# Performance work log

Measured on AMD Instinct MI355X. Metric: run time of the kernel, lower is better.

The kernel has to match this reference:

```python
import jax, jax.numpy as jnp
import numpy as np

D_IN = 4096
NUM_HEADS = 32
NUM_KV_GROUPS = 8
HEAD_DIM = D_IN // NUM_HEADS  # 128 (init overwrites head_dim)
GROUP_SIZE = NUM_HEADS // NUM_KV_GROUPS
SEQ = 2048
BATCH = 1
EPS = 1e-6


def layernorm(t, w, b):
    mu = jnp.mean(t, axis=-1, keepdims=True)
    var = jnp.var(t, axis=-1, keepdims=True)
    return (t - mu) * jax.lax.rsqrt(var + EPS) * w + b


def rope(t, cos, sin):
    # t: [B, H, S, D]; cos/sin: [S, D] broadcast over B, H
    half = t.shape[-1] // 2
    x1, x2 = t[..., :half], t[..., half:]
    rot = jnp.concatenate([-x2, x1], axis=-1)
    return t * cos + rot * sin


def setup_inputs() -> dict:
    key = jax.random.key(0)
    ks = jax.random.split(key, 10)
    x = jax.random.normal(ks[0], (BATCH, SEQ, D_IN), dtype=jnp.float32)
    mask = jnp.triu(jnp.ones((SEQ, SEQ), dtype=bool), k=1)  # True = masked (causal)
    # RoPE tables
    inv_freq = 1.0 / (10000.0 ** (np.arange(0, HEAD_DIM, 2, dtype=np.float32) / HEAD_DIM))
    pos = np.arange(SEQ, dtype=np.float32)
    ang = np.einsum('s,d->sd', pos, inv_freq)  # [S, D/2]
    ang = np.concatenate([ang, ang], axis=-1)  # [S, D]
    cos = jnp.asarray(np.cos(ang))
    sin = jnp.asarray(np.sin(ang))
    s = 0.02
    Wq = jax.random.normal(ks[1], (D_IN, NUM_HEADS * HEAD_DIM), dtype=jnp.float32) * s
    Wk = jax.random.normal(ks[2], (D_IN, NUM_KV_GROUPS * HEAD_DIM), dtype=jnp.float32) * s
    Wv = jax.random.normal(ks[3], (D_IN, NUM_KV_GROUPS * HEAD_DIM), dtype=jnp.float32) * s
    Wo = jax.random.normal(ks[4], (NUM_HEADS * HEAD_DIM, D_IN), dtype=jnp.float32) * s
    qn_w = jnp.ones((HEAD_DIM,), jnp.float32)
    qn_b = jnp.zeros((HEAD_DIM,), jnp.float32)
    kn_w = jnp.ones((HEAD_DIM,), jnp.float32)
    kn_b = jnp.zeros((HEAD_DIM,), jnp.float32)
    return {"x": x, "mask": mask, "cos": cos, "sin": sin, "Wq": Wq, "Wk": Wk,
            "Wv": Wv, "Wo": Wo, "qn_w": qn_w, "qn_b": qn_b, "kn_w": kn_w, "kn_b": kn_b}


def reference(x, mask, cos, sin, Wq, Wk, Wv, Wo, qn_w, qn_b, kn_w, kn_b):
    B, S, _ = x.shape
    q = (x @ Wq).reshape(B, S, NUM_HEADS, HEAD_DIM).transpose(0, 2, 1, 3)      # [B,H,S,D]
    k = (x @ Wk).reshape(B, S, NUM_KV_GROUPS, HEAD_DIM).transpose(0, 2, 1, 3)  # [B,G,S,D]
    v = (x @ Wv).reshape(B, S, NUM_KV_GROUPS, HEAD_DIM).transpose(0, 2, 1, 3)
    q = layernorm(q, qn_w, qn_b)
    k = layernorm(k, kn_w, kn_b)
    q = rope(q, cos, sin)
    k = rope(k, cos, sin)
    k = jnp.repeat(k, GROUP_SIZE, axis=1)  # [B,H,S,D]
    v = jnp.repeat(v, GROUP_SIZE, axis=1)
    scores = jnp.einsum('bhqd,bhkd->bhqk', q, k)
    scores = jnp.where(mask, -jnp.inf, scores)
    attn = jax.nn.softmax(scores / jnp.sqrt(jnp.float32(HEAD_DIM)), axis=-1)
    ctx = jnp.einsum('bhqk,bhkd->bhqd', attn, v)
    ctx = ctx.transpose(0, 2, 1, 3).reshape(B, S, NUM_HEADS * HEAD_DIM)
    return ctx @ Wo
```

## Files before the change

kernel.cpp:

```cpp
#include <hip/hip_runtime.h>
#include <stdint.h>

#define SQ   2048
#define DIN  4096
#define NH   32
#define NKV  8
#define HD   128
#define NQKV 6144

typedef float f32x4 __attribute__((ext_vector_type(4)));
typedef short bf16x8 __attribute__((ext_vector_type(8)));

__device__ __forceinline__ short f2bf(float f) {
  union { float f; uint32_t u; } v; v.f = f;
  uint32_t r = (v.u + 0x7FFFu + ((v.u >> 16) & 1u)) >> 16;
  return (short)r;
}

__device__ __forceinline__ void gl2lds(const void* g, void* l) {
  __builtin_amdgcn_global_load_lds(
      (const __attribute__((address_space(1))) void*)g,
      (__attribute__((address_space(3))) void*)l, 16, 0, 0);
}

__global__ void cvt_bf16(const float* __restrict__ src, short* __restrict__ dst, long n) {
  long i = ((long)blockIdx.x * blockDim.x + threadIdx.x) * 4;
  if (i + 3 < n) {
    float4 v = *(const float4*)(src + i);
    short o[4] = { f2bf(v.x), f2bf(v.y), f2bf(v.z), f2bf(v.w) };
    *(uint2*)(dst + i) = *(uint2*)o;
  }
}

__global__ __launch_bounds__(256) void transpose_cvt(const float* __restrict__ src, int ldS, long zS,
                                                     short* __restrict__ dst, int ldD, long zD) {
  __shared__ float tile[64][65];
  src += (long)blockIdx.z * zS;
  dst += (long)blockIdx.z * zD;
  int r0 = blockIdx.y * 64, c0 = blockIdx.x * 64;
  int tid = threadIdx.x;
#pragma unroll
  for (int i = 0; i < 16; ++i) {
    int idx = i * 256 + tid;
    int rr = idx >> 6, cc = idx & 63;
    tile[rr][cc] = src[(long)(r0 + rr) * ldS + c0 + cc];
  }
  __syncthreads();
#pragma unroll
  for (int i = 0; i < 16; ++i) {
    int idx = i * 256 + tid;
    int dr = idx >> 6, dc = idx & 63;
    dst[(long)(c0 + dr) * ldD + r0 + dc] = f2bf(tile[dc][dr]);
  }
}

#define BM 128
#define BN 128
#define BK 32
__global__ __launch_bounds__(256) void gemm_bf16(const short* __restrict__ A, const short* __restrict__ Bt,
                                                 float* __restrict__ C, int M, int N, int K) {
  __shared__ __align__(16) short As[BM * BK];
  __shared__ __align__(16) short Bs[BN * BK];
  int tid = threadIdx.x;
  int wave = tid >> 6, lane = tid & 63;
  int l16 = lane & 15, lq = lane >> 4;
  int m0 = blockIdx.y * BM, n0 = blockIdx.x * BN;
  int wm = (wave >> 1) * 64, wn = (wave & 1) * 64;
  int ch = (lane & 3) ^ ((lane >> 3) & 3);
  f32x4 acc[4][4] = {};
  for (int k0 = 0; k0 < K; k0 += BK) {
#pragma unroll
    for (int c = 0; c < 2; ++c) {
      int call = wave * 2 + c;
      int r = call * 16 + (lane >> 2);
      gl2lds(&A[(long)(m0 + r) * K + k0 + ch * 8], &As[call * 512]);
      gl2lds(&Bt[(long)(n0 + r) * K + k0 + ch * 8], &Bs[call * 512]);
    }
    __syncthreads();
    bf16x8 af[4], bfr[4];
#pragma unroll
    for (int i = 0; i < 4; ++i) {
      int row = wm + i * 16 + l16;
      af[i] = *(const bf16x8*)&As[row * BK + (lq ^ ((row >> 1) & 3)) * 8];
    }
#pragma unroll
    for (int j = 0; j < 4; ++j) {
      int row = wn + j * 16 + l16;
      bfr[j] = *(const bf16x8*)&Bs[row * BK + (lq ^ ((row >> 1) & 3)) * 8];
    }
#pragma unroll
    for (int i = 0; i < 4; ++i)
#pragma unroll
      for (int j = 0; j < 4; ++j)
        acc[i][j] = __builtin_amdgcn_mfma_f32_16x16x32_bf16(af[i], bfr[j], acc[i][j], 0, 0, 0);
    __syncthreads();
  }
#pragma unroll
  for (int i = 0; i < 4; ++i)
#pragma unroll
    for (int j = 0; j < 4; ++j)
#pragma unroll
      for (int r = 0; r < 4; ++r) {
        int row = m0 + wm + i * 16 + lq * 4 + r;
        int col = n0 + wn + j * 16 + l16;
        C[(long)row * N + col] = acc[i][j][r];
      }
}

__global__ __launch_bounds__(64) void ln_rope(const float* __restrict__ qkv,
                                              const float* __restrict__ cosb, const float* __restrict__ sinb,
                                              const float* __restrict__ qw, const float* __restrict__ qb,
                                              const float* __restrict__ kw, const float* __restrict__ kb,
                                              short* __restrict__ qo, short* __restrict__ ko) {
  int s = blockIdx.x, slice = blockIdx.y, t = threadIdx.x;
  bool isq = slice < NH;
  int off = isq ? slice * HD : DIN + (slice - NH) * HD;
  const float* src = qkv + (long)s * NQKV + off;
  float v0 = src[t], v1 = src[t + 64];
  float sum = v0 + v1, ss = v0 * v0 + v1 * v1;
#pragma unroll
  for (int o = 1; o < 64; o <<= 1) { sum += __shfl_xor(sum, o); ss += __shfl_xor(ss, o); }
  float mu = sum * (1.f / 128.f);
  float var = ss * (1.f / 128.f) - mu * mu;
  float rstd = rsqrtf(var + 1e-6f);
  const float* w  = isq ? qw : kw;
  const float* bb = isq ? qb : kb;
  float n0 = (v0 - mu) * rstd * w[t]      + bb[t];
  float n1 = (v1 - mu) * rstd * w[t + 64] + bb[t + 64];
  float c0 = cosb[s * HD + t], c1 = cosb[s * HD + t + 64];
  float s0 = sinb[s * HD + t], s1 = sinb[s * HD + t + 64];
  float o0 = n0 * c0 - n1 * s0;
  float o1 = n1 * c1 + n0 * s1;
  short* dst = isq ? (qo + ((long)slice * SQ + s) * HD)
                   : (ko + ((long)(slice - NH) * SQ + s) * HD);
  dst[t] = f2bf(o0);
  dst[t + 64] = f2bf(o1);
}

__global__ __launch_bounds__(256) void attn(const short* __restrict__ q, const short* __restrict__ k,
                                            const short* __restrict__ vT, short* __restrict__ ctx) {
  int pair = blockIdx.x, h = blockIdx.y, g = h >> 2;
  int tid = threadIdx.x, w = tid >> 6, lane = tid & 63;
  int l16 = lane & 15, lq = lane >> 4;
  __shared__ __align__(16) short Ks[64 * 128];
  __shared__ __align__(16) short Vs[128 * 64];
  __shared__ __align__(16) short pbuf[4][16 * 72];
  const short* qh = q + (long)h * SQ * HD;
  const short* kg = k + (long)g * SQ * HD;
  const short* vg = vT + (long)g * HD * SQ;
  int kr = (w * 4) * 4 + (lane >> 4);
  int vrw = (w * 4) * 8 + (lane >> 3);
  const float sc = 0.08838834764831845f * 1.4426950408889634f;

  for (int st = 0; st < 2; ++st) {
    int qt = st ? (31 - pair) : pair;
    int qbase = qt * 64 + w * 16;
    bf16x8 aq[4];
#pragma unroll
    for (int kk = 0; kk < 4; ++kk)
      aq[kk] = *(const bf16x8*)&qh[(long)(qbase + l16) * HD + kk * 32 + lq * 8];
    float m_r[4], l_r[4];
    f32x4 acc[8] = {};
#pragma unroll
    for (int r = 0; r < 4; ++r) { m_r[r] = -__builtin_inff(); l_r[r] = 0.f; }

    for (int kt = 0; kt <= qt; ++kt) {
#pragma unroll
      for (int j = 0; j < 4; ++j) {
        int call = w * 4 + j;
        int r = kr + j * 4;
        int chk = (lane & 15) ^ (r & 15);
        gl2lds(&kg[(long)(kt * 64 + r) * HD + chk * 8], &Ks[call * 512]);
        int rv = vrw + j * 8;
        int chv = (lane & 7) ^ (rv & 7);
        gl2lds(&vg[(long)rv * SQ + kt * 64 + chv * 8], &Vs[call * 512]);
      }
      __syncthreads();
      f32x4 s4[4];
#pragma unroll
      for (int b = 0; b < 4; ++b) s4[b] = (f32x4){0.f, 0.f, 0.f, 0.f};
#pragma unroll
      for (int b = 0; b < 4; ++b) {
        int krow = b * 16 + l16;
#pragma unroll
        for (int kk = 0; kk < 4; ++kk) {
          bf16x8 bk = *(const bf16x8*)&Ks[krow * 128 + ((kk * 4 + lq) ^ (krow & 15)) * 8];
          s4[b] = __builtin_amdgcn_mfma_f32_16x16x32_bf16(aq[kk], bk, s4[b], 0, 0, 0);
        }
      }
      int qrow0 = qbase + lq * 4;
#pragma unroll
      for (int b = 0; b < 4; ++b) {
        int key = kt * 64 + b * 16 + l16;
#pragma unroll
        for (int r = 0; r < 4; ++r) {
          float val = s4[b][r] * sc;
          s4[b][r] = (key > qrow0 + r) ? -__builtin_inff() : val;
        }
      }
      float p[4][4];
#pragma unroll
      for (int r = 0; r < 4; ++r) {
        float mx = fmaxf(fmaxf(s4[0][r], s4[1][r]), fmaxf(s4[2][r], s4[3][r]));
#pragma unroll
        for (int o = 1; o < 16; o <<= 1) mx = fmaxf(mx, __shfl_xor(mx, o));
        float mnew = fmaxf(m_r[r], mx);
        float alpha = exp2f(m_r[r] - mnew);
        float sum = 0.f;
#pragma unroll
        for (int b = 0; b < 4; ++b) { float pv = exp2f(s4[b][r] - mnew); p[b][r] = pv; sum += pv; }
#pragma unroll
        for (int o = 1; o < 16; o <<= 1) sum += __shfl_xor(sum, o);
        l_r[r] = l_r[r] * alpha + sum;
        m_r[r] = mnew;
#pragma unroll
        for (int n = 0; n < 8; ++n) acc[n][r] *= alpha;
      }
#pragma unroll
      for (int b = 0; b < 4; ++b)
#pragma unroll
        for (int r = 0; r < 4; ++r)
          pbuf[w][(lq * 4 + r) * 72 + b * 16 + l16] = f2bf(p[b][r]);
#pragma unroll
      for (int kk = 0; kk < 2; ++kk) {
        bf16x8 pf = *(const bf16x8*)&pbuf[w][l16 * 72 + kk * 32 + lq * 8];
#pragma unroll
        for (int n = 0; n < 8; ++n) {
          int vrow = n * 16 + l16;
          bf16x8 vf = *(const bf16x8*)&Vs[vrow * 64 + ((kk * 4 + lq) ^ (vrow & 7)) * 8];
          acc[n] = __builtin_amdgcn_mfma_f32_16x16x32_bf16(pf, vf, acc[n], 0, 0, 0);
        }
      }
      __syncthreads();
    }
#pragma unroll
    for (int n = 0; n < 8; ++n)
#pragma unroll
      for (int r = 0; r < 4; ++r) {
        int srow = qbase + lq * 4 + r;
        ctx[(long)srow * (NH * HD) + h * HD + n * 16 + l16] = f2bf(acc[n][r] / l_r[r]);
      }
  }
}

#define XB_OFF     0L
#define QR_OFF     0L
#define WQKVT_OFF  16777216L
#define KR_OFF     16777216L
#define VT_OFF     20971520L
#define CTX_OFF    25165824L
#define WOT_OFF    67108864L
#define QKV_OFF    100663296L

extern "C" void kernel_launch(void* const* d_in, const int* in_sizes, int n_in,
                              void* d_out, int out_size, void* d_ws, size_t ws_size,
                              hipStream_t stream) {
  const float* x    = (const float*)d_in[0];
  const float* cosb = (const float*)d_in[2];
  const float* sinb = (const float*)d_in[3];
  const float* Wq   = (const float*)d_in[4];
  const float* Wk   = (const float*)d_in[5];
  const float* Wv   = (const float*)d_in[6];
  const float* Wo   = (const float*)d_in[7];
  const float* qnw  = (const float*)d_in[8];
  const float* qnb  = (const float*)d_in[9];
  const float* knw  = (const float*)d_in[10];
  const float* knb  = (const float*)d_in[11];

  char* ws = (char*)d_ws;
  short* xb    = (short*)(ws + XB_OFF);
  short* qr    = (short*)(ws + QR_OFF);
  short* wqkvt = (short*)(ws + WQKVT_OFF);
  short* krp   = (short*)(ws + KR_OFF);
  short* vt    = (short*)(ws + VT_OFF);
  short* ctx   = (short*)(ws + CTX_OFF);
  short* wot   = (short*)(ws + WOT_OFF);
  float* qkv   = (float*)(ws + QKV_OFF);

  cvt_bf16<<<8192, 256, 0, stream>>>(x, xb, (long)SQ * DIN);
  transpose_cvt<<<dim3(64, 64, 1), 256, 0, stream>>>(Wq, 4096, 0L, wqkvt, 4096, 0L);
  transpose_cvt<<<dim3(16, 64, 1), 256, 0, stream>>>(Wk, 1024, 0L, wqkvt + (long)4096 * 4096, 4096, 0L);
  transpose_cvt<<<dim3(16, 64, 1), 256, 0, stream>>>(Wv, 1024, 0L, wqkvt + (long)5120 * 4096, 4096, 0L);
  transpose_cvt<<<dim3(64, 64, 1), 256, 0, stream>>>(Wo, 4096, 0L, wot, 4096, 0L);
  gemm_bf16<<<dim3(NQKV / BN, SQ / BM), 256, 0, stream>>>(xb, wqkvt, qkv, SQ, NQKV, DIN);
  ln_rope<<<dim3(SQ, NH + NKV), 64, 0, stream>>>(qkv, cosb, sinb, qnw, qnb, knw, knb, qr, krp);
  transpose_cvt<<<dim3(2, 32, 8), 256, 0, stream>>>(qkv + 5120, NQKV, 128L, vt, SQ, (long)HD * SQ);
  attn<<<dim3(16, NH), 256, 0, stream>>>(qr, krp, vt, ctx);
  gemm_bf16<<<dim3(DIN / BN, SQ / BM), 256, 0, stream>>>(ctx, wot, (float*)d_out, SQ, DIN, DIN);
}
```

Measured before the change: 609.9 us.

## Fuse LayerNorm, RoPE and V transpose into QKV GEMM epilogue; restructure attention

```diff
diff --git a/kernel.cpp b/kernel.cpp
--- a/kernel.cpp
+++ b/kernel.cpp
@@ -57,6 +57,112 @@
 #define BM 128
 #define BN 128
 #define BK 32
+
+__global__ __launch_bounds__(256) void gemm_qkv(const short* __restrict__ A, const short* __restrict__ Bt,
+                                                const float* __restrict__ cosb, const float* __restrict__ sinb,
+                                                const float* __restrict__ qw, const float* __restrict__ qb,
+                                                const float* __restrict__ kw, const float* __restrict__ kb,
+                                                short* __restrict__ qo, short* __restrict__ ko,
+                                                short* __restrict__ vo) {
+  __shared__ __align__(16) short smem[8704];
+  short* As = smem;
+  short* Bs = smem + 4096;
+  const int K = DIN;
+  int tid = threadIdx.x, wave = tid >> 6, lane = tid & 63;
+  int l16 = lane & 15, lq = lane >> 4;
+  int m0 = blockIdx.y * BM;
+  int cb = blockIdx.x;
+  long n0 = (long)cb * BN;
+  int wm = wave * 32;
+  int ch = (lane & 3) ^ ((lane >> 3) & 3);
+  f32x4 acc[2][8] = {};
+  for (int k0 = 0; k0 < K; k0 += BK) {
+#pragma unroll
+    for (int c = 0; c < 2; ++c) {
+      int call = wave * 2 + c;
+      int r = call * 16 + (lane >> 2);
+      gl2lds(&A[(long)(m0 + r) * K + k0 + ch * 8], &As[call * 512]);
+      gl2lds(&Bt[(n0 + r) * K + k0 + ch * 8], &Bs[call * 512]);
+    }
+    __syncthreads();
+    bf16x8 af[2], bfr[8];
+#pragma unroll
+    for (int i = 0; i < 2; ++i) {
+      int row = wm + i * 16 + l16;
+      af[i] = *(const bf16x8*)&As[row * BK + (lq ^ ((row >> 1) & 3)) * 8];
+    }
+#pragma unroll
+    for (int j = 0; j < 8; ++j) {
+      int row = j * 16 + l16;
+      bfr[j] = *(const bf16x8*)&Bs[row * BK + (lq ^ ((row >> 1) & 3)) * 8];
+    }
+#pragma unroll
+    for (int i = 0; i < 2; ++i)
+#pragma unroll
+      for (int j = 0; j < 8; ++j)
+        acc[i][j] = __builtin_amdgcn_mfma_f32_16x16x32_bf16(af[i], bfr[j], acc[i][j], 0, 0, 0);
+    __syncthreads();
+  }
+  if (cb < 40) {
+    bool isq = cb < NH;
+    const float* lw = isq ? qw : kw;
+    const float* lb = isq ? qb : kb;
+    float wv[8], bv[8];
+#pragma unroll
+    for (int j = 0; j < 8; ++j) { wv[j] = lw[j * 16 + l16]; bv[j] = lb[j * 16 + l16]; }
+    short* dst = isq ? (qo + (long)cb * SQ * HD) : (ko + (long)(cb - 32) * SQ * HD);
+#pragma unroll
+    for (int i = 0; i < 2; ++i)
+#pragma unroll
+      for (int r = 0; r < 4; ++r) {
+        int s = m0 + wm + i * 16 + lq * 4 + r;
+        float s1 = 0.f, s2 = 0.f;
+#pragma unroll
+        for (int j = 0; j < 8; ++j) { float v = acc[i][j][r]; s1 += v; s2 += v * v; }
+#pragma unroll
+        for (int o = 1; o < 16; o <<= 1) { s1 += __shfl_xor(s1, o); s2 += __shfl_xor(s2, o); }
+        float mu = s1 * (1.f / 128.f);
+        float rstd = rsqrtf(s2 * (1.f / 128.f) - mu * mu + 1e-6f);
+        float val[8];
+#pragma unroll
+        for (int j = 0; j < 8; ++j) val[j] = (acc[i][j][r] - mu) * rstd * wv[j] + bv[j];
+#pragma unroll
+        for (int j = 0; j < 4; ++j) {
+          int d = j * 16 + l16;
+          float c = cosb[(long)s * HD + d];
+          float sn = sinb[(long)s * HD + d];
+          dst[(long)s * HD + d]      = f2bf(val[j] * c - val[j + 4] * sn);
+          dst[(long)s * HD + d + 64] = f2bf(val[j + 4] * c + val[j] * sn);
+        }
+      }
+  } else {
+    short* vdst = vo + (long)(cb - 40) * HD * SQ;
+#pragma unroll
+    for (int p = 0; p < 2; ++p) {
+      __syncthreads();
+#pragma unroll
+      for (int i = 0; i < 2; ++i)
+#pragma unroll
+        for (int j = 0; j < 4; ++j) {
+          int dl = j * 16 + l16;
+#pragma unroll
+          for (int r = 0; r < 4; ++r) {
+            int sl = wm + i * 16 + lq * 4 + r;
+            smem[dl * 136 + sl] = f2bf(acc[i][p * 4 + j][r]);
+          }
+        }
+      __syncthreads();
+#pragma unroll
+      for (int c = 0; c < 4; ++c) {
+        int idx = c * 256 + tid;
+        int drow = idx >> 4, off = (idx & 15) * 8;
+        uint4 v = *(const uint4*)&smem[drow * 136 + off];
+        *(uint4*)&vdst[(long)(p * 64 + drow) * SQ + m0 + off] = v;
+      }
+    }
+  }
+}
+
 __global__ __launch_bounds__(256) void gemm_bf16(const short* __restrict__ A, const short* __restrict__ Bt,
                                                  float* __restrict__ C, int M, int N, int K) {
   __shared__ __align__(16) short As[BM * BK];
@@ -107,150 +213,149 @@
       }
 }
 
-__global__ __launch_bounds__(64) void ln_rope(const float* __restrict__ qkv,
-                                              const float* __restrict__ cosb, const float* __restrict__ sinb,
-                                              const float* __restrict__ qw, const float* __restrict__ qb,
-                                              const float* __restrict__ kw, const float* __restrict__ kb,
-                                              short* __restrict__ qo, short* __restrict__ ko) {
-  int s = blockIdx.x, slice = blockIdx.y, t = threadIdx.x;
-  bool isq = slice < NH;
-  int off = isq ? slice * HD : DIN + (slice - NH) * HD;
-  const float* src = qkv + (long)s * NQKV + off;
-  float v0 = src[t], v1 = src[t + 64];
-  float sum = v0 + v1, ss = v0 * v0 + v1 * v1;
-#pragma unroll
-  for (int o = 1; o < 64; o <<= 1) { sum += __shfl_xor(sum, o); ss += __shfl_xor(ss, o); }
-  float mu = sum * (1.f / 128.f);
-  float var = ss * (1.f / 128.f) - mu * mu;
-  float rstd = rsqrtf(var + 1e-6f);
-  const float* w  = isq ? qw : kw;
-  const float* bb = isq ? qb : kb;
-  float n0 = (v0 - mu) * rstd * w[t]      + bb[t];
-  float n1 = (v1 - mu) * rstd * w[t + 64] + bb[t + 64];
-  float c0 = cosb[s * HD + t], c1 = cosb[s * HD + t + 64];
-  float s0 = sinb[s * HD + t], s1 = sinb[s * HD + t + 64];
-  float o0 = n0 * c0 - n1 * s0;
-  float o1 = n1 * c1 + n0 * s1;
-  short* dst = isq ? (qo + ((long)slice * SQ + s) * HD)
-                   : (ko + ((long)(slice - NH) * SQ + s) * HD);
-  dst[t] = f2bf(o0);
-  dst[t + 64] = f2bf(o1);
-}
-
-__global__ __launch_bounds__(256) void attn(const short* __restrict__ q, const short* __restrict__ k,
-                                            const short* __restrict__ vT, short* __restrict__ ctx) {
+#define NEG_INF (-__builtin_inff())
+
+template<int NB, bool MASK>
+__device__ __forceinline__ void score_tile(const short* Ks, const bf16x8* aq,
+                                           float* p, float* m, float* l, f32x4* acc,
+                                           int key0, int qrow0, int l16, int lq, float sc) {
+  f32x4 s4[NB];
+#pragma unroll
+  for (int b = 0; b < NB; ++b) {
+    f32x4 t = {0.f, 0.f, 0.f, 0.f};
+#pragma unroll
+    for (int kk = 0; kk < 4; ++kk) {
+      bf16x8 bk = *(const bf16x8*)&Ks[(b * 16 + l16) * 128 + (((kk * 4 + lq) ^ l16) * 8)];
+      t = __builtin_amdgcn_mfma_f32_16x16x32_bf16(aq[kk], bk, t, 0, 0, 0);
+    }
+    if (MASK) {
+      int key = key0 + b * 16 + l16;
+#pragma unroll
+      for (int r = 0; r < 4; ++r) t[r] = (key > qrow0 + r) ? NEG_INF : t[r] * sc;
+    } else {
+#pragma unroll
+      for (int r = 0; r < 4; ++r) t[r] = t[r] * sc;
+    }
+    s4[b] = t;
+  }
+#pragma unroll
+  for (int r = 0; r < 4; ++r) {
+    float mx = s4[0][r];
+#pragma unroll
+    for (int b = 1; b < NB; ++b) mx = fmaxf(mx, s4[b][r]);
+#pragma unroll
+    for (int o = 1; o < 16; o <<= 1) mx = fmaxf(mx, __shfl_xor(mx, o));
+    float mnew = fmaxf(m[r], mx);
+    float alpha = exp2f(m[r] - mnew);
+    float sum = 0.f;
+#pragma unroll
+    for (int b = 0; b < NB; ++b) { float pv = exp2f(s4[b][r] - mnew); p[b * 4 + r] = pv; sum += pv; }
+#pragma unroll
+    for (int o = 1; o < 16; o <<= 1) sum += __shfl_xor(sum, o);
+    l[r] = l[r] * alpha + sum;
+    m[r] = mnew;
+#pragma unroll
+    for (int n = 0; n < 8; ++n) acc[n][r] *= alpha;
+  }
+}
+
+template<int NB>
+__device__ __forceinline__ void pv_tile(short* pbuf, const short* Vs, const float* p,
+                                        f32x4* acc, int l16, int lq) {
+#pragma unroll
+  for (int b = 0; b < NB; ++b)
+#pragma unroll
+    for (int r = 0; r < 4; ++r)
+      pbuf[(lq * 4 + r) * 136 + b * 16 + l16] = f2bf(p[b * 4 + r]);
+#pragma unroll
+  for (int kk = 0; kk < NB / 2; ++kk) {
+    bf16x8 pf = *(const bf16x8*)&pbuf[l16 * 136 + kk * 32 + lq * 8];
+#pragma unroll
+    for (int n = 0; n < 8; ++n) {
+      bf16x8 vf = *(const bf16x8*)&Vs[(n * 16 + l16) * 128 + (((kk * 4 + lq) ^ l16) * 8)];
+      acc[n] = __builtin_amdgcn_mfma_f32_16x16x32_bf16(pf, vf, acc[n], 0, 0, 0);
+    }
+  }
+}
+
+__global__ __launch_bounds__(256, 2) void attn(const short* __restrict__ q, const short* __restrict__ k,
+                                               const short* __restrict__ vT, short* __restrict__ ctx) {
   int pair = blockIdx.x, h = blockIdx.y, g = h >> 2;
   int tid = threadIdx.x, w = tid >> 6, lane = tid & 63;
   int l16 = lane & 15, lq = lane >> 4;
-  __shared__ __align__(16) short Ks[64 * 128];
-  __shared__ __align__(16) short Vs[128 * 64];
-  __shared__ __align__(16) short pbuf[4][16 * 72];
+  __shared__ __align__(16) short Ks[128 * 128];
+  __shared__ __align__(16) short Vs[128 * 128];
+  short* pbuf = Ks + w * 2176;
   const short* qh = q + (long)h * SQ * HD;
   const short* kg = k + (long)g * SQ * HD;
   const short* vg = vT + (long)g * HD * SQ;
-  int kr = (w * 4) * 4 + (lane >> 4);
-  int vrw = (w * 4) * 8 + (lane >> 3);
+  int qtA = pair, qtB = 31 - pair;
+  int ktmaxA = qtA >> 1, ktmaxB = qtB >> 1;
   const float sc = 0.08838834764831845f * 1.4426950408889634f;
 
-  for (int st = 0; st < 2; ++st) {
-    int qt = st ? (31 - pair) : pair;
-    int qbase = qt * 64 + w * 16;
-    bf16x8 aq[4];
-#pragma unroll
-    for (int kk = 0; kk < 4; ++kk)
-      aq[kk] = *(const bf16x8*)&qh[(long)(qbase + l16) * HD + kk * 32 + lq * 8];
-    float m_r[4], l_r[4];
-    f32x4 acc[8] = {};
-#pragma unroll
-    for (int r = 0; r < 4; ++r) { m_r[r] = -__builtin_inff(); l_r[r] = 0.f; }
-
-    for (int kt = 0; kt <= qt; ++kt) {
-#pragma unroll
-      for (int j = 0; j < 4; ++j) {
-        int call = w * 4 + j;
-        int r = kr + j * 4;
-        int chk = (lane & 15) ^ (r & 15);
-        gl2lds(&kg[(long)(kt * 64 + r) * HD + chk * 8], &Ks[call * 512]);
-        int rv = vrw + j * 8;
-        int chv = (lane & 7) ^ (rv & 7);
-        gl2lds(&vg[(long)rv * SQ + kt * 64 + chv * 8], &Vs[call * 512]);
-      }
-      __syncthreads();
-      f32x4 s4[4];
-#pragma unroll
-      for (int b = 0; b < 4; ++b) s4[b] = (f32x4){0.f, 0.f, 0.f, 0.f};
-#pragma unroll
-      for (int b = 0; b < 4; ++b) {
-        int krow = b * 16 + l16;
-#pragma unroll
-        for (int kk = 0; kk < 4; ++kk) {
-          bf16x8 bk = *(const bf16x8*)&Ks[krow * 128 + ((kk * 4 + lq) ^ (krow & 15)) * 8];
-          s4[b] = __builtin_amdgcn_mfma_f32_16x16x32_bf16(aq[kk], bk, s4[b], 0, 0, 0);
-        }
-      }
-      int qrow0 = qbase + lq * 4;
-#pragma unroll
-      for (int b = 0; b < 4; ++b) {
-        int key = kt * 64 + b * 16 + l16;
-#pragma unroll
-        for (int r = 0; r < 4; ++r) {
-          float val = s4[b][r] * sc;
-          s4[b][r] = (key > qrow0 + r) ? -__builtin_inff() : val;
-        }
-      }
-      float p[4][4];
-#pragma unroll
-      for (int r = 0; r < 4; ++r) {
-        float mx = fmaxf(fmaxf(s4[0][r], s4[1][r]), fmaxf(s4[2][r], s4[3][r]));
-#pragma unroll
-        for (int o = 1; o < 16; o <<= 1) mx = fmaxf(mx, __shfl_xor(mx, o));
-        float mnew = fmaxf(m_r[r], mx);
-        float alpha = exp2f(m_r[r] - mnew);
-        float sum = 0.f;
-#pragma unroll
-        for (int b = 0; b < 4; ++b) { float pv = exp2f(s4[b][r] - mnew); p[b][r] = pv; sum += pv; }
-#pragma unroll
-        for (int o = 1; o < 16; o <<= 1) sum += __shfl_xor(sum, o);
-        l_r[r] = l_r[r] * alpha + sum;
-        m_r[r] = mnew;
-#pragma unroll
-        for (int n = 0; n < 8; ++n) acc[n][r] *= alpha;
-      }
-#pragma unroll
-      for (int b = 0; b < 4; ++b)
-#pragma unroll
-        for (int r = 0; r < 4; ++r)
-          pbuf[w][(lq * 4 + r) * 72 + b * 16 + l16] = f2bf(p[b][r]);
-#pragma unroll
-      for (int kk = 0; kk < 2; ++kk) {
-        bf16x8 pf = *(const bf16x8*)&pbuf[w][l16 * 72 + kk * 32 + lq * 8];
-#pragma unroll
-        for (int n = 0; n < 8; ++n) {
-          int vrow = n * 16 + l16;
-          bf16x8 vf = *(const bf16x8*)&Vs[vrow * 64 + ((kk * 4 + lq) ^ (vrow & 7)) * 8];
-          acc[n] = __builtin_amdgcn_mfma_f32_16x16x32_bf16(pf, vf, acc[n], 0, 0, 0);
-        }
-      }
-      __syncthreads();
-    }
-#pragma unroll
-    for (int n = 0; n < 8; ++n)
-#pragma unroll
-      for (int r = 0; r < 4; ++r) {
-        int srow = qbase + lq * 4 + r;
-        ctx[(long)srow * (NH * HD) + h * HD + n * 16 + l16] = f2bf(acc[n][r] / l_r[r]);
-      }
-  }
+  bf16x8 aqA[4], aqB[4];
+#pragma unroll
+  for (int kk = 0; kk < 4; ++kk) {
+    aqA[kk] = *(const bf16x8*)&qh[(long)(qtA * 64 + w * 16 + l16) * HD + kk * 32 + lq * 8];
+    aqB[kk] = *(const bf16x8*)&qh[(long)(qtB * 64 + w * 16 + l16) * HD + kk * 32 + lq * 8];
+  }
+  float mA[4], lA[4], mB[4], lB[4];
+  f32x4 accA[8] = {}, accB[8] = {};
+#pragma unroll
+  for (int r = 0; r < 4; ++r) { mA[r] = NEG_INF; lA[r] = 0.f; mB[r] = NEG_INF; lB[r] = 0.f; }
+  int qrowA = qtA * 64 + w * 16 + lq * 4;
+  int qrowB = qtB * 64 + w * 16 + lq * 4;
+  float pA[32], pB[32];
+
+  for (int kt = 0; kt <= ktmaxB; ++kt) {
+    __syncthreads();
+#pragma unroll
+    for (int j = 0; j < 8; ++j) {
+      int call = w * 8 + j;
+      int r = call * 4 + (lane >> 4);
+      int chk = (lane & 15) ^ (r & 15);
+      gl2lds(&kg[(long)(kt * 128 + r) * HD + chk * 8], &Ks[call * 512]);
+      gl2lds(&vg[(long)r * SQ + kt * 128 + chk * 8], &Vs[call * 512]);
+    }
+    __syncthreads();
+    bool doA = (kt <= ktmaxA);
+    int nbB = 8, nbA = 8;
+    if (kt == ktmaxB && !(qtB & 1)) nbB = 4;
+    if (kt == ktmaxA && !(qtA & 1)) nbA = 4;
+    if (kt == ktmaxB) {
+      if (nbB == 8) score_tile<8, true>(Ks, aqB, pB, mB, lB, accB, kt * 128, qrowB, l16, lq, sc);
+      else          score_tile<4, true>(Ks, aqB, pB, mB, lB, accB, kt * 128, qrowB, l16, lq, sc);
+    } else          score_tile<8, false>(Ks, aqB, pB, mB, lB, accB, kt * 128, qrowB, l16, lq, sc);
+    if (doA) {
+      if (kt == ktmaxA) {
+        if (nbA == 8) score_tile<8, true>(Ks, aqA, pA, mA, lA, accA, kt * 128, qrowA, l16, lq, sc);
+        else          score_tile<4, true>(Ks, aqA, pA, mA, lA, accA, kt * 128, qrowA, l16, lq, sc);
+      } else          score_tile<8, false>(Ks, aqA, pA, mA, lA, accA, kt * 128, qrowA, l16, lq, sc);
+    }
+    __syncthreads();
+    if (nbB == 8) pv_tile<8>(pbuf, Vs, pB, accB, l16, lq);
+    else          pv_tile<4>(pbuf, Vs, pB, accB, l16, lq);
+    if (doA) {
+      if (nbA == 8) pv_tile<8>(pbuf, Vs, pA, accA, l16, lq);
+      else          pv_tile<4>(pbuf, Vs, pA, accA, l16, lq);
+    }
+  }
+#pragma unroll
+  for (int n = 0; n < 8; ++n)
+#pragma unroll
+    for (int r = 0; r < 4; ++r) {
+      ctx[(long)(qrowA + r) * (NH * HD) + h * HD + n * 16 + l16] = f2bf(accA[n][r] / lA[r]);
+      ctx[(long)(qrowB + r) * (NH * HD) + h * HD + n * 16 + l16] = f2bf(accB[n][r] / lB[r]);
+    }
 }
 
 #define XB_OFF     0L
-#define QR_OFF     0L
+#define CTX_OFF    0L
 #define WQKVT_OFF  16777216L
-#define KR_OFF     16777216L
-#define VT_OFF     20971520L
-#define CTX_OFF    25165824L
 #define WOT_OFF    67108864L
-#define QKV_OFF    100663296L
+#define QR_OFF     100663296L
+#define KR_OFF     117440512L
+#define VT_OFF     121634816L
 
 extern "C" void kernel_launch(void* const* d_in, const int* in_sizes, int n_in,
                               void* d_out, int out_size, void* d_ws, size_t ws_size,
@@ -269,22 +374,20 @@
 
   char* ws = (char*)d_ws;
   short* xb    = (short*)(ws + XB_OFF);
+  short* ctx   = (short*)(ws + CTX_OFF);
+  short* wqkvt = (short*)(ws + WQKVT_OFF);
+  short* wot   = (short*)(ws + WOT_OFF);
   short* qr    = (short*)(ws + QR_OFF);
-  short* wqkvt = (short*)(ws + WQKVT_OFF);
   short* krp   = (short*)(ws + KR_OFF);
   short* vt    = (short*)(ws + VT_OFF);
-  short* ctx   = (short*)(ws + CTX_OFF);
-  short* wot   = (short*)(ws + WOT_OFF);
-  float* qkv   = (float*)(ws + QKV_OFF);
 
   cvt_bf16<<<8192, 256, 0, stream>>>(x, xb, (long)SQ * DIN);
   transpose_cvt<<<dim3(64, 64, 1), 256, 0, stream>>>(Wq, 4096, 0L, wqkvt, 4096, 0L);
   transpose_cvt<<<dim3(16, 64, 1), 256, 0, stream>>>(Wk, 1024, 0L, wqkvt + (long)4096 * 4096, 4096, 0L);
   transpose_cvt<<<dim3(16, 64, 1), 256, 0, stream>>>(Wv, 1024, 0L, wqkvt + (long)5120 * 4096, 4096, 0L);
   transpose_cvt<<<dim3(64, 64, 1), 256, 0, stream>>>(Wo, 4096, 0L, wot, 4096, 0L);
-  gemm_bf16<<<dim3(NQKV / BN, SQ / BM), 256, 0, stream>>>(xb, wqkvt, qkv, SQ, NQKV, DIN);
-  ln_rope<<<dim3(SQ, NH + NKV), 64, 0, stream>>>(qkv, cosb, sinb, qnw, qnb, knw, knb, qr, krp);
-  transpose_cvt<<<dim3(2, 32, 8), 256, 0, stream>>>(qkv + 5120, NQKV, 128L, vt, SQ, (long)HD * SQ);
+  gemm_qkv<<<dim3(NQKV / BN, SQ / BM), 256, 0, stream>>>(xb, wqkvt, cosb, sinb,
+                                                         qnw, qnb, knw, knb, qr, krp, vt);
   attn<<<dim3(16, NH), 256, 0, stream>>>(qr, krp, vt, ctx);
   gemm_bf16<<<dim3(DIN / BN, SQ / BM), 256, 0, stream>>>(ctx, wot, (float*)d_out, SQ, DIN, DIN);
 }
```

Measured after the change: 692.3 us. +13.5%, slower.

## Rewrite attention with 32x32 MFMA, register-resident P, per-wave strips, no LDS

Applied to the files above, without the earlier changes.

```diff
diff --git a/kernel.cpp b/kernel.cpp
--- a/kernel.cpp
+++ b/kernel.cpp
@@ -8,13 +8,17 @@
 #define HD   128
 #define NQKV 6144
 
-typedef float f32x4 __attribute__((ext_vector_type(4)));
+typedef float f32x4  __attribute__((ext_vector_type(4)));
+typedef float f32x16 __attribute__((ext_vector_type(16)));
 typedef short bf16x8 __attribute__((ext_vector_type(8)));
 
 __device__ __forceinline__ short f2bf(float f) {
   union { float f; uint32_t u; } v; v.f = f;
   uint32_t r = (v.u + 0x7FFFu + ((v.u >> 16) & 1u)) >> 16;
   return (short)r;
+}
+__device__ __forceinline__ uint32_t pack2bf(float a, float b) {
+  return (uint32_t)(uint16_t)f2bf(a) | ((uint32_t)(uint16_t)f2bf(b) << 16);
 }
 
 __device__ __forceinline__ void gl2lds(const void* g, void* l) {
@@ -137,109 +141,138 @@
   dst[t + 64] = f2bf(o1);
 }
 
-__global__ __launch_bounds__(256) void attn(const short* __restrict__ q, const short* __restrict__ k,
-                                            const short* __restrict__ vT, short* __restrict__ ctx) {
-  int pair = blockIdx.x, h = blockIdx.y, g = h >> 2;
-  int tid = threadIdx.x, w = tid >> 6, lane = tid & 63;
-  int l16 = lane & 15, lq = lane >> 4;
-  __shared__ __align__(16) short Ks[64 * 128];
-  __shared__ __align__(16) short Vs[128 * 64];
-  __shared__ __align__(16) short pbuf[4][16 * 72];
+#define NEG_INF (-__builtin_inff())
+
+__device__ __forceinline__ void attn_step(const short* __restrict__ kg, const short* __restrict__ vg,
+                                          const bf16x8* aq, int kt, int qlo, int l32, int pm,
+                                          bool last, float& m, float& l, f32x16* acc) {
+  const float sc = 0.08838834764831845f * 1.4426950408889634f;
+  bool do1 = !last || (qlo & 32);
+  bool mask0 = last && !(qlo & 32);
+  bool mask1 = last && (qlo & 32);
+  int q = qlo + l32;
+  f32x16 s0 = {}, s1 = {};
+#pragma unroll
+  for (int t = 0; t < 8; ++t) {
+    bf16x8 kf = *(const bf16x8*)&kg[(long)(kt * 64 + l32) * HD + t * 16 + pm * 8];
+    s0 = __builtin_amdgcn_mfma_f32_32x32x16_bf16(kf, aq[t], s0, 0, 0, 0);
+  }
+  if (do1) {
+#pragma unroll
+    for (int t = 0; t < 8; ++t) {
+      bf16x8 kf = *(const bf16x8*)&kg[(long)(kt * 64 + 32 + l32) * HD + t * 16 + pm * 8];
+      s1 = __builtin_amdgcn_mfma_f32_32x32x16_bf16(kf, aq[t], s1, 0, 0, 0);
+    }
+  }
+#pragma unroll
+  for (int i = 0; i < 16; ++i) {
+    float v = s0[i] * sc;
+    if (mask0) { int key = kt * 64 + (i & 3) + 8 * (i >> 2) + 4 * pm; v = (key > q) ? NEG_INF : v; }
+    s0[i] = v;
+  }
+  if (do1) {
+#pragma unroll
+    for (int i = 0; i < 16; ++i) {
+      float v = s1[i] * sc;
+      if (mask1) { int key = kt * 64 + 32 + (i & 3) + 8 * (i >> 2) + 4 * pm; v = (key > q) ? NEG_INF : v; }
+      s1[i] = v;
+    }
+  }
+  float mx = s0[0];
+#pragma unroll
+  for (int i = 1; i < 16; ++i) mx = fmaxf(mx, s0[i]);
+  if (do1) {
+#pragma unroll
+    for (int i = 0; i < 16; ++i) mx = fmaxf(mx, s1[i]);
+  }
+  mx = fmaxf(mx, __shfl_xor(mx, 32));
+  float mnew = fmaxf(m, mx);
+  float alpha = exp2f(m - mnew);
+  float sum = 0.f;
+  uint32_t pk0[8], pk1[8];
+#pragma unroll
+  for (int i = 0; i < 8; ++i) {
+    float a = exp2f(s0[2 * i] - mnew), b = exp2f(s0[2 * i + 1] - mnew);
+    sum += a + b;
+    pk0[i] = pack2bf(a, b);
+  }
+  if (do1) {
+#pragma unroll
+    for (int i = 0; i < 8; ++i) {
+      float a = exp2f(s1[2 * i] - mnew), b = exp2f(s1[2 * i + 1] - mnew);
+      sum += a + b;
+      pk1[i] = pack2bf(a, b);
+    }
+  }
+  sum += __shfl_xor(sum, 32);
+  l = l * alpha + sum;
+  m = mnew;
+#pragma unroll
+  for (int db = 0; db < 4; ++db)
+#pragma unroll
+    for (int i = 0; i < 16; ++i) acc[db][i] *= alpha;
+#pragma unroll
+  for (int ks = 0; ks < 4; ++ks) {
+    if (ks < 2 || do1) {
+      int a = ks & 1;
+      uint32_t x0 = (ks >> 1) ? pk1[4 * a + 0] : pk0[4 * a + 0];
+      uint32_t x1 = (ks >> 1) ? pk1[4 * a + 1] : pk0[4 * a + 1];
+      uint32_t x2 = (ks >> 1) ? pk1[4 * a + 2] : pk0[4 * a + 2];
+      uint32_t x3 = (ks >> 1) ? pk1[4 * a + 3] : pk0[4 * a + 3];
+      uint32_t own0 = pm ? x2 : x0, own1 = pm ? x3 : x1;
+      uint32_t snd0 = pm ? x0 : x2, snd1 = pm ? x1 : x3;
+      uint32_t r0 = (uint32_t)__shfl_xor((int)snd0, 32);
+      uint32_t r1 = (uint32_t)__shfl_xor((int)snd1, 32);
+      union { uint32_t u[4]; bf16x8 v; } pf;
+      pf.u[0] = pm ? r0 : own0;  pf.u[1] = pm ? r1 : own1;
+      pf.u[2] = pm ? own0 : r0;  pf.u[3] = pm ? own1 : r1;
+#pragma unroll
+      for (int db = 0; db < 4; ++db) {
+        bf16x8 vf = *(const bf16x8*)&vg[(long)(db * 32 + l32) * SQ + kt * 64 + ks * 16 + pm * 8];
+        acc[db] = __builtin_amdgcn_mfma_f32_32x32x16_bf16(vf, pf.v, acc[db], 0, 0, 0);
+      }
+    }
+  }
+}
+
+__global__ __launch_bounds__(256, 2) void attn(const short* __restrict__ q, const short* __restrict__ k,
+                                               const short* __restrict__ vT, short* __restrict__ ctx) {
+  int b = blockIdx.x;
+  int g = b & 7;
+  int h = g * 4 + ((b >> 3) & 3);
+  int w = threadIdx.x >> 6, lane = threadIdx.x & 63;
+  int l32 = lane & 31, pm = lane >> 5;
+  int strip = (15 - (b >> 5)) * 4 + w;
+  int qlo = strip * 32;
   const short* qh = q + (long)h * SQ * HD;
   const short* kg = k + (long)g * SQ * HD;
   const short* vg = vT + (long)g * HD * SQ;
-  int kr = (w * 4) * 4 + (lane >> 4);
-  int vrw = (w * 4) * 8 + (lane >> 3);
-  const float sc = 0.08838834764831845f * 1.4426950408889634f;
-
-  for (int st = 0; st < 2; ++st) {
-    int qt = st ? (31 - pair) : pair;
-    int qbase = qt * 64 + w * 16;
-    bf16x8 aq[4];
-#pragma unroll
-    for (int kk = 0; kk < 4; ++kk)
-      aq[kk] = *(const bf16x8*)&qh[(long)(qbase + l16) * HD + kk * 32 + lq * 8];
-    float m_r[4], l_r[4];
-    f32x4 acc[8] = {};
-#pragma unroll
-    for (int r = 0; r < 4; ++r) { m_r[r] = -__builtin_inff(); l_r[r] = 0.f; }
-
-    for (int kt = 0; kt <= qt; ++kt) {
-#pragma unroll
-      for (int j = 0; j < 4; ++j) {
-        int call = w * 4 + j;
-        int r = kr + j * 4;
-        int chk = (lane & 15) ^ (r & 15);
-        gl2lds(&kg[(long)(kt * 64 + r) * HD + chk * 8], &Ks[call * 512]);
-        int rv = vrw + j * 8;
-        int chv = (lane & 7) ^ (rv & 7);
-        gl2lds(&vg[(long)rv * SQ + kt * 64 + chv * 8], &Vs[call * 512]);
-      }
-      __syncthreads();
-      f32x4 s4[4];
-#pragma unroll
-      for (int b = 0; b < 4; ++b) s4[b] = (f32x4){0.f, 0.f, 0.f, 0.f};
-#pragma unroll
-      for (int b = 0; b < 4; ++b) {
-        int krow = b * 16 + l16;
-#pragma unroll
-        for (int kk = 0; kk < 4; ++kk) {
-          bf16x8 bk = *(const bf16x8*)&Ks[krow * 128 + ((kk * 4 + lq) ^ (krow & 15)) * 8];
-          s4[b] = __builtin_amdgcn_mfma_f32_16x16x32_bf16(aq[kk], bk, s4[b], 0, 0, 0);
-        }
-      }
-      int qrow0 = qbase + lq * 4;
-#pragma unroll
-      for (int b = 0; b < 4; ++b) {
-        int key = kt * 64 + b * 16 + l16;
-#pragma unroll
-        for (int r = 0; r < 4; ++r) {
-          float val = s4[b][r] * sc;
-          s4[b][r] = (key > qrow0 + r) ? -__builtin_inff() : val;
-        }
-      }
-      float p[4][4];
-#pragma unroll
-      for (int r = 0; r < 4; ++r) {
-        float mx = fmaxf(fmaxf(s4[0][r], s4[1][r]), fmaxf(s4[2][r], s4[3][r]));
-#pragma unroll
-        for (int o = 1; o < 16; o <<= 1) mx = fmaxf(mx, __shfl_xor(mx, o));
-        float mnew = fmaxf(m_r[r], mx);
-        float alpha = exp2f(m_r[r] - mnew);
-        float sum = 0.f;
-#pragma unroll
-        for (int b = 0; b < 4; ++b) { float pv = exp2f(s4[b][r] - mnew); p[b][r] = pv; sum += pv; }
-#pragma unroll
-        for (int o = 1; o < 16; o <<= 1) sum += __shfl_xor(sum, o);
-        l_r[r] = l_r[r] * alpha + sum;
-        m_r[r] = mnew;
-#pragma unroll
-        for (int n = 0; n < 8; ++n) acc[n][r] *= alpha;
-      }
-#pragma unroll
-      for (int b = 0; b < 4; ++b)
-#pragma unroll
-        for (int r = 0; r < 4; ++r)
-          pbuf[w][(lq * 4 + r) * 72 + b * 16 + l16] = f2bf(p[b][r]);
-#pragma unroll
-      for (int kk = 0; kk < 2; ++kk) {
-        bf16x8 pf = *(const bf16x8*)&pbuf[w][l16 * 72 + kk * 32 + lq * 8];
-#pragma unroll
-        for (int n = 0; n < 8; ++n) {
-          int vrow = n * 16 + l16;
-          bf16x8 vf = *(const bf16x8*)&Vs[vrow * 64 + ((kk * 4 + lq) ^ (vrow & 7)) * 8];
-          acc[n] = __builtin_amdgcn_mfma_f32_16x16x32_bf16(pf, vf, acc[n], 0, 0, 0);
-        }
-      }
-      __syncthreads();
-    }
-#pragma unroll
-    for (int n = 0; n < 8; ++n)
-#pragma unroll
-      for (int r = 0; r < 4; ++r) {
-        int srow = qbase + lq * 4 + r;
-        ctx[(long)srow * (NH * HD) + h * HD + n * 16 + l16] = f2bf(acc[n][r] / l_r[r]);
-      }
+  bf16x8 aq[8];
+#pragma unroll
+  for (int t = 0; t < 8; ++t)
+    aq[t] = *(const bf16x8*)&qh[(long)(qlo + l32) * HD + t * 16 + pm * 8];
+  float m = NEG_INF, l = 0.f;
+  f32x16 acc[4] = {};
+  int nkt = ((qlo + 31) >> 6) + 1;
+  for (int kt = 0; kt < nkt; ++kt)
+    attn_step(kg, vg, aq, kt, qlo, l32, pm, kt == nkt - 1, m, l, acc);
+  float inv = 1.0f / l;
+#pragma unroll
+  for (int db = 0; db < 4; ++db) {
+    uint32_t ou[8];
+#pragma unroll
+    for (int i = 0; i < 8; ++i)
+      ou[i] = pack2bf(acc[db][2 * i] * inv, acc[db][2 * i + 1] * inv);
+#pragma unroll
+    for (int c = 0; c < 4; ++c) {
+      uint32_t o0 = ou[2 * c], o1 = ou[2 * c + 1];
+      uint32_t r0 = (uint32_t)__shfl_xor((int)o0, 32);
+      uint32_t r1 = (uint32_t)__shfl_xor((int)o1, 32);
+      uint4 st;
+      st.x = pm ? r0 : o0;  st.y = pm ? r1 : o1;
+      st.z = pm ? o0 : r0;  st.w = pm ? o1 : r1;
+      *(uint4*)&ctx[(long)(qlo + l32) * DIN + h * HD + db * 32 + c * 8] = st;
+    }
   }
 }
 
@@ -285,6 +318,6 @@
   gemm_bf16<<<dim3(NQKV / BN, SQ / BM), 256, 0, stream>>>(xb, wqkvt, qkv, SQ, NQKV, DIN);
   ln_rope<<<dim3(SQ, NH + NKV), 64, 0, stream>>>(qkv, cosb, sinb, qnw, qnb, knw, knb, qr, krp);
   transpose_cvt<<<dim3(2, 32, 8), 256, 0, stream>>>(qkv + 5120, NQKV, 128L, vt, SQ, (long)HD * SQ);
-  attn<<<dim3(16, NH), 256, 0, stream>>>(qr, krp, vt, ctx);
+  attn<<<dim3(512), 256, 0, stream>>>(qr, krp, vt, ctx);
   gemm_bf16<<<dim3(DIN / BN, SQ / BM), 256, 0, stream>>>(ctx, wot, (float*)d_out, SQ, DIN, DIN);
 }
```

After: 705.8 us. +15.7%, slower.
